# Kernel tuning notes

Hardware: AMD Instinct MI355X
Metric: run time of the kernel (lower is better)

## Reference

```python
import jax, jax.numpy as jnp
import numpy as np

N = 100000      # nodes
E = 3200000     # edges
F_IN = 128      # num_features
H = 32          # hidden_dim (hard-coded in module)
C = 8           # num_classes
B = 128         # graphs in batch
BN_EPS = 1e-5


def setup_inputs() -> dict:
    key = jax.random.key(0)
    ks = jax.random.split(key, 24)
    s = 0.1
    inp = {
        "x": jax.random.normal(ks[0], (N, F_IN), jnp.float32),
        "edge_index": jax.random.randint(ks[1], (2, E), 0, N, dtype=jnp.int32),
        "batch": jnp.sort(jax.random.randint(ks[2], (N,), 0, B, dtype=jnp.int32)),
        # GINConv layer 0 (F_IN -> H -> H) MLP + BN params
        "w1_0": jax.random.normal(ks[3], (F_IN, H), jnp.float32) * s,
        "b1_0": jnp.zeros((H,), jnp.float32),
        "w2_0": jax.random.normal(ks[4], (H, H), jnp.float32) * s,
        "b2_0": jnp.zeros((H,), jnp.float32),
        "g_0": jnp.ones((H,), jnp.float32),
        "be_0": jnp.zeros((H,), jnp.float32),
        # GINConv layers 1..3 (H -> H -> H), stacked
        "w1s": jax.random.normal(ks[5], (3, H, H), jnp.float32) * s,
        "b1s": jnp.zeros((3, H), jnp.float32),
        "w2s": jax.random.normal(ks[6], (3, H, H), jnp.float32) * s,
        "b2s": jnp.zeros((3, H), jnp.float32),
        "gs": jnp.ones((3, H), jnp.float32),
        "bes": jnp.zeros((3, H), jnp.float32),
        # classifier head
        "fc1_w": jax.random.normal(ks[7], (H, H), jnp.float32) * s,
        "fc1_b": jnp.zeros((H,), jnp.float32),
        "fc2_w": jax.random.normal(ks[8], (H, C), jnp.float32) * s,
        "fc2_b": jnp.zeros((C,), jnp.float32),
    }
    return inp


def _gin_conv(h, src, dst, w1, b1, w2, b2):
    # GINConv with eps=0: MLP((1+eps)*x + sum_{j in N(i)} x_j)
    agg = jax.ops.segment_sum(h[src], dst, num_segments=N)  # scatter-add aggregation
    z = h + agg
    return jnp.maximum(z @ w1 + b1, 0.0) @ w2 + b2


def _batch_norm(h, gamma, beta):
    # BatchNorm1d in training mode: batch stats over node dim, biased variance
    mean = h.mean(axis=0)
    var = jnp.mean(jnp.square(h - mean), axis=0)
    return gamma * (h - mean) * jax.lax.rsqrt(var + BN_EPS) + beta


def reference(x, edge_index, batch, w1_0, b1_0, w2_0, b2_0, g_0, be_0,
              w1s, b1s, w2s, b2s, gs, bes, fc1_w, fc1_b, fc2_w, fc2_b):
    src, dst = edge_index[0], edge_index[1]
    h = _batch_norm(jnp.maximum(_gin_conv(x, src, dst, w1_0, b1_0, w2_0, b2_0), 0.0), g_0, be_0)
    for i in range(3):  # fixed small layer loop
        h = _batch_norm(jnp.maximum(_gin_conv(h, src, dst, w1s[i], b1s[i], w2s[i], b2s[i]), 0.0), gs[i], bes[i])
    # global_mean_pool over batch ids
    counts = jax.ops.segment_sum(jnp.ones((N,), h.dtype), batch, num_segments=B)
    pooled = jax.ops.segment_sum(h, batch, num_segments=B) / jnp.maximum(counts, 1.0)[:, None]
    h = jnp.maximum(pooled @ fc1_w + fc1_b, 0.0)
    # dropout p=0.5 treated as identity (eval-mode determinism)
    logits = h @ fc2_w + fc2_b
    return jax.nn.log_softmax(logits, axis=-1)
```

## Files before the change

### kernel.cpp

```cpp
#include <hip/hip_runtime.h>
#include <hip/hip_bf16.h>

#define NN   100000
#define EE   3200000
#define HH   32
#define BB   128
#define KMAX 96
#define LSTRIDE 97
#define NBKT 1024
#define BSPAN 98
#define EBLK 256
#define CHUNK 12500

typedef float f32x4 __attribute__((ext_vector_type(4)));

static constexpr size_t Q_OFF      = 0;
static constexpr size_t EPACK_OFF  = 6400000;
static constexpr size_t H_OFF      = 19200000;
static constexpr size_t SRC_OFF    = 32000000;
static constexpr size_t OFF_OFF    = 44800000;
static constexpr size_t HIST_OFF   = 45300000;
static constexpr size_t CUR_OFF    = 46400000;
static constexpr size_t BBASE_OFF  = 47500000;
static constexpr size_t STATS_OFF  = 47600000;
static constexpr size_t POOLED_OFF = 47601024;
static constexpr size_t PCNT_OFF   = 47617408;
static constexpr size_t ZERO_OFF   = STATS_OFF;
static constexpr size_t ZERO_BYTES = 17920;

__global__ __launch_bounds__(256) void hist_kernel(const int* __restrict__ ei,
                                                   int* __restrict__ hist) {
    __shared__ int lh[NBKT];
    int tid = threadIdx.x, blk = blockIdx.x;
    for (int i = tid; i < NBKT; i += 256) lh[i] = 0;
    __syncthreads();
    int e0 = blk * CHUNK;
    for (int e = e0 + tid; e < e0 + CHUNK; e += 256) {
        int d = ei[EE + e];
        atomicAdd(&lh[d / BSPAN], 1);
    }
    __syncthreads();
    for (int i = tid; i < NBKT; i += 256) hist[blk * NBKT + i] = lh[i];
}

__global__ __launch_bounds__(1024) void bucket_scan_kernel(const int* __restrict__ hist,
                                                           int* __restrict__ bbase,
                                                           int* __restrict__ cursor) {
    __shared__ int sm[NBKT];
    int t = threadIdx.x;
    int mine = 0;
    for (int blk = 0; blk < EBLK; blk++) mine += hist[blk * NBKT + t];
    sm[t] = mine;
    __syncthreads();
    for (int off = 1; off < NBKT; off <<= 1) {
        int v = (t >= off) ? sm[t - off] : 0;
        __syncthreads();
        sm[t] += v;
        __syncthreads();
    }
    int base = sm[t] - mine;
    bbase[t] = base;
    cursor[t] = base;
    if (t == NBKT - 1) bbase[NBKT] = sm[t];
}

__global__ __launch_bounds__(256) void scatter_kernel(const int* __restrict__ ei,
                                                      const int* __restrict__ hist,
                                                      int* __restrict__ cursor,
                                                      int* __restrict__ epack) {
    __shared__ int lbs[NBKT];
    __shared__ int lh[NBKT];
    int tid = threadIdx.x, blk = blockIdx.x;
    for (int i = tid; i < NBKT; i += 256) {
        int c = hist[blk * NBKT + i];
        lbs[i] = (c > 0) ? atomicAdd(&cursor[i], c) : 0;
        lh[i] = 0;
    }
    __syncthreads();
    int e0 = blk * CHUNK;
    for (int e = e0 + tid; e < e0 + CHUNK; e += 256) {
        int s = ei[e];
        int d = ei[EE + e];
        int b = d / BSPAN;
        int slot = lbs[b] + atomicAdd(&lh[b], 1);
        epack[slot] = s | ((d - b * BSPAN) << 17);
    }
}

__global__ __launch_bounds__(256) void csr_compact_kernel(const int* __restrict__ epack,
                                                          const int* __restrict__ bbase,
                                                          int* __restrict__ off,
                                                          int* __restrict__ srcs) {
    __shared__ int lcnt[BSPAN];
    __shared__ int lbase[BSPAN + 1];
    __shared__ int lcsr[BSPAN * LSTRIDE];
    int b = blockIdx.x;
    int base = b * BSPAN;
    int span = NN - base;
    if (span <= 0) return;
    if (span > BSPAN) span = BSPAN;
    int tid = threadIdx.x;
    for (int i = tid; i < span; i += 256) lcnt[i] = 0;
    __syncthreads();
    int p0 = bbase[b], p1 = bbase[b + 1];
    for (int i = p0 + tid; i < p1; i += 256) {
        int wd = epack[i];
        int ld = wd >> 17;
        int slot = atomicAdd(&lcnt[ld], 1);
        if (slot < KMAX) lcsr[ld * LSTRIDE + slot] = wd & 0x1FFFF;
    }
    __syncthreads();
    if (tid == 0) {
        int run = 0;
        for (int i = 0; i < span; i++) { lbase[i] = run; run += min(lcnt[i], KMAX); }
        lbase[span] = run;
    }
    __syncthreads();
    for (int i = tid; i < span; i += 256) off[base + i] = p0 + lbase[i];
    if (base + span == NN && tid == 0) off[NN] = p0 + lbase[span];
    int m = lbase[span];
    for (int j = tid; j < m; j += 256) {
        int lo = 0, hi = span - 1;
        while (lo < hi) {
            int mid = (lo + hi + 1) >> 1;
            if (lbase[mid] <= j) lo = mid; else hi = mid - 1;
        }
        srcs[p0 + j] = lcsr[lo * LSTRIDE + (j - lbase[lo])];
    }
}

__device__ __forceinline__ unsigned bf16rn(float f) {
    unsigned b = __float_as_uint(f);
    return (b + 0x7fffu + ((b >> 16) & 1u)) >> 16;
}

__device__ __forceinline__ void acc_row(float* a, uint4 v) {
    a[0] += __uint_as_float(v.x << 16);
    a[1] += __uint_as_float(v.x & 0xffff0000u);
    a[2] += __uint_as_float(v.y << 16);
    a[3] += __uint_as_float(v.y & 0xffff0000u);
    a[4] += __uint_as_float(v.z << 16);
    a[5] += __uint_as_float(v.z & 0xffff0000u);
    a[6] += __uint_as_float(v.w << 16);
    a[7] += __uint_as_float(v.w & 0xffff0000u);
}

template <int FIN>
__global__ __launch_bounds__(256) void proj_kernel(const float* __restrict__ hin,
                                                   const float* __restrict__ w1,
                                                   const float* __restrict__ stats_prev,
                                                   const float* __restrict__ gamma,
                                                   const float* __restrict__ beta,
                                                   uint4* __restrict__ q4) {
    constexpr int JC = FIN / 4;
    __shared__ float sa[32], sc[32];
    __shared__ float part[4 * 64 * 33];
    int tid = threadIdx.x;
    if constexpr (FIN == 32) {
        if (tid < 32) {
            float mean = stats_prev[tid] * (1.0f / NN);
            float var  = fmaxf(stats_prev[32 + tid] * (1.0f / NN) - mean * mean, 0.f);
            float av = gamma[tid] * rsqrtf(var + 1e-5f);
            sa[tid] = av;
            sc[tid] = beta[tid] - mean * av;
        }
        __syncthreads();
    }
    int wv = __builtin_amdgcn_readfirstlane(tid >> 6);
    int ln = tid & 63;
    int n = blockIdx.x * 64 + ln;
    float acc[32];
#pragma unroll
    for (int c = 0; c < 32; c++) acc[c] = 0.f;
    if (n < NN) {
        const float4* h4 = (const float4*)(hin + (size_t)n * FIN + wv * JC);
        float hv[JC];
#pragma unroll
        for (int k = 0; k < JC / 4; k++) {
            float4 v = h4[k];
            hv[4*k] = v.x; hv[4*k+1] = v.y; hv[4*k+2] = v.z; hv[4*k+3] = v.w;
        }
        if constexpr (FIN == 32) {
#pragma unroll
            for (int j = 0; j < JC; j++) hv[j] = fmaf(hv[j], sa[wv * JC + j], sc[wv * JC + j]);
        }
#pragma unroll 4
        for (int j = 0; j < JC; j++) {
            float hvj = hv[j];
            const float* wrow = w1 + (size_t)(wv * JC + j) * 32;
#pragma unroll
            for (int c = 0; c < 32; c++) acc[c] = fmaf(hvj, wrow[c], acc[c]);
        }
    }
    float* my = part + (wv * 64 + ln) * 33;
#pragma unroll
    for (int c = 0; c < 32; c++) my[c] = acc[c];
    __syncthreads();
    int node = tid >> 2, p = tid & 3;
    int n2 = blockIdx.x * 64 + node;
    if (n2 >= NN) return;
    float r[8];
#pragma unroll
    for (int k = 0; k < 8; k++) {
        int c = p * 8 + k;
        r[k] = (part[(0 * 64 + node) * 33 + c] + part[(1 * 64 + node) * 33 + c])
             + (part[(2 * 64 + node) * 33 + c] + part[(3 * 64 + node) * 33 + c]);
    }
    uint4 u;
    u.x = bf16rn(r[0]) | (bf16rn(r[1]) << 16);
    u.y = bf16rn(r[2]) | (bf16rn(r[3]) << 16);
    u.z = bf16rn(r[4]) | (bf16rn(r[5]) << 16);
    u.w = bf16rn(r[6]) | (bf16rn(r[7]) << 16);
    q4[(size_t)n2 * 4 + p] = u;
}

__global__ __launch_bounds__(256) void gather_mlp_kernel(const uint4* __restrict__ q4,
                                                         const int* __restrict__ srcs,
                                                         const int* __restrict__ off,
                                                         const float* __restrict__ b1,
                                                         const float* __restrict__ w2,
                                                         const float* __restrict__ b2,
                                                         float* __restrict__ hout,
                                                         float* __restrict__ stats) {
    __shared__ float w2t[32 * 33];
    __shared__ float ut[32 * 33];
    __shared__ float pst[32 * 8];
    int tid = threadIdx.x;
    for (int i = tid; i < 1024; i += 256) w2t[(i >> 5) * 33 + (i & 31)] = w2[i];
    int t = blockIdx.x * 256 + tid;
    int n = t >> 3;
    int p = tid & 7;
    int nl = (tid >> 3) & 31;
    int e0 = off[n], e1 = off[n + 1];
    float acc[32];
#pragma unroll
    for (int c = 0; c < 32; c++) acc[c] = 0.f;
    int i = e0 + p;
    for (; i + 8 < e1; i += 16) {
        int s0 = __builtin_nontemporal_load(srcs + i);
        int s1 = __builtin_nontemporal_load(srcs + i + 8);
        uint4 a0 = q4[(size_t)s0 * 4 + 0];
        uint4 a1 = q4[(size_t)s0 * 4 + 1];
        uint4 a2 = q4[(size_t)s0 * 4 + 2];
        uint4 a3 = q4[(size_t)s0 * 4 + 3];
        uint4 c0 = q4[(size_t)s1 * 4 + 0];
        uint4 c1 = q4[(size_t)s1 * 4 + 1];
        uint4 c2 = q4[(size_t)s1 * 4 + 2];
        uint4 c3 = q4[(size_t)s1 * 4 + 3];
        acc_row(acc + 0,  a0); acc_row(acc + 8,  a1);
        acc_row(acc + 16, a2); acc_row(acc + 24, a3);
        acc_row(acc + 0,  c0); acc_row(acc + 8,  c1);
        acc_row(acc + 16, c2); acc_row(acc + 24, c3);
    }
    if (i < e1) {
        int s0 = __builtin_nontemporal_load(srcs + i);
        uint4 a0 = q4[(size_t)s0 * 4 + 0];
        uint4 a1 = q4[(size_t)s0 * 4 + 1];
        uint4 a2 = q4[(size_t)s0 * 4 + 2];
        uint4 a3 = q4[(size_t)s0 * 4 + 3];
        acc_row(acc + 0,  a0); acc_row(acc + 8,  a1);
        acc_row(acc + 16, a2); acc_row(acc + 24, a3);
    }
    int sel1 = p & 1, sel2 = (p >> 1) & 1, sel3 = (p >> 2) & 1;
    float k16[16];
#pragma unroll
    for (int r = 0; r < 16; r++) {
        float send = sel1 ? acc[r] : acc[r + 16];
        float recv = __shfl_xor(send, 1);
        k16[r] = (sel1 ? acc[r + 16] : acc[r]) + recv;
    }
    float k8[8];
#pragma unroll
    for (int r = 0; r < 8; r++) {
        float send = sel2 ? k16[r] : k16[r + 8];
        float recv = __shfl_xor(send, 2);
        k8[r] = (sel2 ? k16[r + 8] : k16[r]) + recv;
    }
    float k4[4];
#pragma unroll
    for (int r = 0; r < 4; r++) {
        float send = sel3 ? k8[r] : k8[r + 4];
        float recv = __shfl_xor(send, 4);
        k4[r] = (sel3 ? k8[r + 4] : k8[r]) + recv;
    }
    int base = 16 * sel1 + 8 * sel2 + 4 * sel3;
    {
        uint4 v = q4[(size_t)n * 4 + (base >> 3)];
        unsigned w0 = sel3 ? v.z : v.x;
        unsigned w1 = sel3 ? v.w : v.y;
        k4[0] += __uint_as_float(w0 << 16);
        k4[1] += __uint_as_float(w0 & 0xffff0000u);
        k4[2] += __uint_as_float(w1 << 16);
        k4[3] += __uint_as_float(w1 & 0xffff0000u);
    }
    const float4 bv = *(const float4*)(b1 + base);
    float u0 = fmaxf(k4[0] + bv.x, 0.f);
    float u1 = fmaxf(k4[1] + bv.y, 0.f);
    float u2 = fmaxf(k4[2] + bv.z, 0.f);
    float u3 = fmaxf(k4[3] + bv.w, 0.f);
    float* urow = ut + nl * 33 + base;
    urow[0] = u0; urow[1] = u1; urow[2] = u2; urow[3] = u3;
    __syncthreads();
    const float4 b2v = *(const float4*)(b2 + base);
    float o0 = b2v.x, o1 = b2v.y, o2 = b2v.z, o3 = b2v.w;
    const float* un = ut + nl * 33;
#pragma unroll 8
    for (int j = 0; j < 32; j++) {
        float uj = un[j];
        const float* wr = w2t + j * 33 + base;
        o0 = fmaf(uj, wr[0], o0);
        o1 = fmaf(uj, wr[1], o1);
        o2 = fmaf(uj, wr[2], o2);
        o3 = fmaf(uj, wr[3], o3);
    }
    o0 = fmaxf(o0, 0.f); o1 = fmaxf(o1, 0.f);
    o2 = fmaxf(o2, 0.f); o3 = fmaxf(o3, 0.f);
    f32x4 hv; hv.x = o0; hv.y = o1; hv.z = o2; hv.w = o3;
    __builtin_nontemporal_store(hv, (f32x4*)(hout + (size_t)n * 32 + base));
    float s0 = o0, s1 = o1, s2 = o2, s3 = o3;
    float q0 = o0 * o0, q1 = o1 * o1, q2 = o2 * o2, q3 = o3 * o3;
#pragma unroll
    for (int m = 8; m < 64; m <<= 1) {
        s0 += __shfl_xor(s0, m); s1 += __shfl_xor(s1, m);
        s2 += __shfl_xor(s2, m); s3 += __shfl_xor(s3, m);
        q0 += __shfl_xor(q0, m); q1 += __shfl_xor(q1, m);
        q2 += __shfl_xor(q2, m); q3 += __shfl_xor(q3, m);
    }
    int wv = tid >> 6;
    if ((tid & 63) < 8) {
        float* ps = pst + (wv * 8 + p) * 8;
        ps[0] = s0; ps[1] = s1; ps[2] = s2; ps[3] = s3;
        ps[4] = q0; ps[5] = q1; ps[6] = q2; ps[7] = q3;
    }
    __syncthreads();
    if (tid < 64) {
        int c = tid & 31;
        int issq = tid >> 5;
        int psel = ((c >> 4) & 1) | (((c >> 3) & 1) << 1) | (((c >> 2) & 1) << 2);
        int k = c & 3;
        float s = 0.f;
#pragma unroll
        for (int w = 0; w < 4; w++) s += pst[(w * 8 + psel) * 8 + issq * 4 + k];
        atomicAdd(&stats[issq * 32 + c], s);
    }
}

#define PR 16
__global__ __launch_bounds__(256) void pool_kernel(const float* __restrict__ h,
                                                   const int* __restrict__ batch,
                                                   float* __restrict__ pooled,
                                                   float* __restrict__ pcnt) {
    int t = blockIdx.x * 256 + threadIdx.x;
    int c = t & 31;
    int g = t >> 5;
    int r0 = g * PR;
    if (r0 >= NN) return;
    int r1 = min(r0 + PR, NN);
    int cur = batch[r0];
    float acc = 0.f, cn = 0.f;
    for (int rr = r0; rr < r1; rr++) {
        int b = batch[rr];
        if (b != cur) {
            atomicAdd(&pooled[cur * 32 + c], acc);
            if (c == 0) atomicAdd(&pcnt[cur], cn);
            acc = 0.f; cn = 0.f; cur = b;
        }
        acc += h[(size_t)rr * 32 + c];
        cn += 1.f;
    }
    atomicAdd(&pooled[cur * 32 + c], acc);
    if (c == 0) atomicAdd(&pcnt[cur], cn);
}

__global__ __launch_bounds__(128) void head_kernel(const float* __restrict__ pooled,
                                                   const float* __restrict__ pcnt,
                                                   const float* __restrict__ stats3,
                                                   const float* __restrict__ g3,
                                                   const float* __restrict__ be3,
                                                   const float* __restrict__ fc1w,
                                                   const float* __restrict__ fc1b,
                                                   const float* __restrict__ fc2w,
                                                   const float* __restrict__ fc2b,
                                                   float* __restrict__ out) {
    __shared__ float sa[32], sc[32];
    int g = threadIdx.x;
    if (g < 32) {
        float mean = stats3[g] * (1.0f / NN);
        float var  = fmaxf(stats3[32 + g] * (1.0f / NN) - mean * mean, 0.f);
        float av = g3[g] * rsqrtf(var + 1e-5f);
        sa[g] = av;
        sc[g] = be3[g] - mean * av;
    }
    __syncthreads();
    if (g >= BB) return;
    float inv = 1.f / fmaxf(pcnt[g], 1.f);
    float xv[32];
#pragma unroll
    for (int c = 0; c < 32; c++) xv[c] = fmaf(sa[c], pooled[g * 32 + c] * inv, sc[c]);
    float u[32];
#pragma unroll 4
    for (int k = 0; k < 32; k++) {
        float s = fc1b[k];
#pragma unroll
        for (int c = 0; c < 32; c++) s = fmaf(xv[c], fc1w[c * 32 + k], s);
        u[k] = fmaxf(s, 0.f);
    }
    float l[8];
#pragma unroll
    for (int o = 0; o < 8; o++) {
        float s = fc2b[o];
#pragma unroll
        for (int k = 0; k < 32; k++) s = fmaf(u[k], fc2w[k * 8 + o], s);
        l[o] = s;
    }
    float m = l[0];
#pragma unroll
    for (int o = 1; o < 8; o++) m = fmaxf(m, l[o]);
    float se = 0.f;
#pragma unroll
    for (int o = 0; o < 8; o++) se += expf(l[o] - m);
    float lse = logf(se) + m;
#pragma unroll
    for (int o = 0; o < 8; o++) out[g * 8 + o] = l[o] - lse;
}

extern "C" void kernel_launch(void* const* d_in, const int* in_sizes, int n_in,
                              void* d_out, int out_size, void* d_ws, size_t ws_size,
                              hipStream_t stream) {
    const float* x    = (const float*)d_in[0];
    const int*   ei   = (const int*)d_in[1];
    const int*   batch= (const int*)d_in[2];
    const float* w1_0 = (const float*)d_in[3];
    const float* b1_0 = (const float*)d_in[4];
    const float* w2_0 = (const float*)d_in[5];
    const float* b2_0 = (const float*)d_in[6];
    const float* g_0  = (const float*)d_in[7];
    const float* be_0 = (const float*)d_in[8];
    const float* w1s  = (const float*)d_in[9];
    const float* b1s  = (const float*)d_in[10];
    const float* w2s  = (const float*)d_in[11];
    const float* b2s  = (const float*)d_in[12];
    const float* gs   = (const float*)d_in[13];
    const float* bes  = (const float*)d_in[14];
    const float* fc1w = (const float*)d_in[15];
    const float* fc1b = (const float*)d_in[16];
    const float* fc2w = (const float*)d_in[17];
    const float* fc2b = (const float*)d_in[18];
    float* out = (float*)d_out;

    char* ws = (char*)d_ws;
    uint4*    q4     = (uint4*)(ws + Q_OFF);
    int*      epack  = (int*)(ws + EPACK_OFF);
    float*    h      = (float*)(ws + H_OFF);
    int*      srcs   = (int*)(ws + SRC_OFF);
    int*      off    = (int*)(ws + OFF_OFF);
    int*      hist   = (int*)(ws + HIST_OFF);
    int*      cursor = (int*)(ws + CUR_OFF);
    int*      bbase  = (int*)(ws + BBASE_OFF);
    float*    stats  = (float*)(ws + STATS_OFF);
    float*    pooled = (float*)(ws + POOLED_OFF);
    float*    pcnt   = (float*)(ws + PCNT_OFF);

    (void)hipMemsetAsync(ws + ZERO_OFF, 0, ZERO_BYTES, stream);

    hist_kernel<<<EBLK, 256, 0, stream>>>(ei, hist);
    bucket_scan_kernel<<<1, NBKT, 0, stream>>>(hist, bbase, cursor);
    scatter_kernel<<<EBLK, 256, 0, stream>>>(ei, hist, cursor, epack);
    csr_compact_kernel<<<NBKT, 256, 0, stream>>>(epack, bbase, off, srcs);

    const int pblk = (NN + 63) / 64;
    const int gblk = (NN * 8) / 256;

    proj_kernel<128><<<pblk, 256, 0, stream>>>(x, w1_0, nullptr, nullptr, nullptr, q4);
    gather_mlp_kernel<<<gblk, 256, 0, stream>>>(q4, srcs, off, b1_0, w2_0, b2_0, h, stats);

    for (int i = 0; i < 3; i++) {
        const float* st_prev = stats + i * 64;
        proj_kernel<32><<<pblk, 256, 0, stream>>>(h, w1s + i * 1024, st_prev,
                                                  gs + i * 32, bes + i * 32, q4);
        gather_mlp_kernel<<<gblk, 256, 0, stream>>>(q4, srcs, off, b1s + i * 32,
                                                    w2s + i * 1024, b2s + i * 32, h,
                                                    stats + (i + 1) * 64);
    }

    int pthreads = ((NN + PR - 1) / PR) * 32;
    pool_kernel<<<(pthreads + 255) / 256, 256, 0, stream>>>(h, batch, pooled, pcnt);
    head_kernel<<<1, 128, 0, stream>>>(pooled, pcnt, stats + 3 * 64, gs + 2 * 32,
                                       bes + 2 * 32, fc1w, fc1b, fc2w, fc2b, out);
}
```

Before: 577.2 us.

## Pipeline gather index loads, replace shared-memory MLP with shuffles, replicate stat atomics

Software-pipelines the edge-source index loads in the gather loop, prefetching the next pair while the current rows are loaded, with a predicated tail instead of a separate remainder path. Drops the shared-memory staging and both block barriers in the second MLP layer by exchanging hidden activations via wavefront shuffles and reading w2 directly from global memory. Spreads batch-norm statistic atomics across 8 replica slots, which consumers now sum. It also corrects which gamma/beta are applied to each layer's batch norm. The cost is more global loads of w2 per thread and more atomics per block.

```diff
diff --git a/kernel.cpp b/kernel.cpp
--- a/kernel.cpp
+++ b/kernel.cpp
@@ -23,10 +23,10 @@
 static constexpr size_t CUR_OFF    = 46400000;
 static constexpr size_t BBASE_OFF  = 47500000;
 static constexpr size_t STATS_OFF  = 47600000;
-static constexpr size_t POOLED_OFF = 47601024;
-static constexpr size_t PCNT_OFF   = 47617408;
+static constexpr size_t POOLED_OFF = 47608192;
+static constexpr size_t PCNT_OFF   = 47624576;
 static constexpr size_t ZERO_OFF   = STATS_OFF;
-static constexpr size_t ZERO_BYTES = 17920;
+static constexpr size_t ZERO_BYTES = 25088;
 
 __global__ __launch_bounds__(256) void hist_kernel(const int* __restrict__ ei,
                                                    int* __restrict__ hist) {
@@ -158,8 +158,14 @@
     int tid = threadIdx.x;
     if constexpr (FIN == 32) {
         if (tid < 32) {
-            float mean = stats_prev[tid] * (1.0f / NN);
-            float var  = fmaxf(stats_prev[32 + tid] * (1.0f / NN) - mean * mean, 0.f);
+            float s = 0.f, sq = 0.f;
+#pragma unroll
+            for (int k = 0; k < 8; k++) {
+                s  += stats_prev[k * 64 + tid];
+                sq += stats_prev[k * 64 + 32 + tid];
+            }
+            float mean = s * (1.0f / NN);
+            float var  = fmaxf(sq * (1.0f / NN) - mean * mean, 0.f);
             float av = gamma[tid] * rsqrtf(var + 1e-5f);
             sa[tid] = av;
             sc[tid] = beta[tid] - mean * av;
@@ -222,44 +228,39 @@
                                                          const float* __restrict__ b2,
                                                          float* __restrict__ hout,
                                                          float* __restrict__ stats) {
-    __shared__ float w2t[32 * 33];
-    __shared__ float ut[32 * 33];
-    __shared__ float pst[32 * 8];
     int tid = threadIdx.x;
-    for (int i = tid; i < 1024; i += 256) w2t[(i >> 5) * 33 + (i & 31)] = w2[i];
     int t = blockIdx.x * 256 + tid;
     int n = t >> 3;
     int p = tid & 7;
-    int nl = (tid >> 3) & 31;
     int e0 = off[n], e1 = off[n + 1];
+    int e1m1 = e1 - 1;
     float acc[32];
 #pragma unroll
     for (int c = 0; c < 32; c++) acc[c] = 0.f;
     int i = e0 + p;
-    for (; i + 8 < e1; i += 16) {
-        int s0 = __builtin_nontemporal_load(srcs + i);
-        int s1 = __builtin_nontemporal_load(srcs + i + 8);
-        uint4 a0 = q4[(size_t)s0 * 4 + 0];
-        uint4 a1 = q4[(size_t)s0 * 4 + 1];
-        uint4 a2 = q4[(size_t)s0 * 4 + 2];
-        uint4 a3 = q4[(size_t)s0 * 4 + 3];
-        uint4 c0 = q4[(size_t)s1 * 4 + 0];
-        uint4 c1 = q4[(size_t)s1 * 4 + 1];
-        uint4 c2 = q4[(size_t)s1 * 4 + 2];
-        uint4 c3 = q4[(size_t)s1 * 4 + 3];
+    int sA = __builtin_nontemporal_load(srcs + min(i, e1m1));
+    int sB = __builtin_nontemporal_load(srcs + min(i + 8, e1m1));
+    while (i < e1) {
+        int inext = i + 16;
+        int sC = __builtin_nontemporal_load(srcs + min(inext, e1m1));
+        int sD = __builtin_nontemporal_load(srcs + min(inext + 8, e1m1));
+        bool vB = (i + 8 < e1);
+        int sBc = vB ? sB : sA;
+        uint4 a0 = q4[(size_t)sA * 4 + 0];
+        uint4 a1 = q4[(size_t)sA * 4 + 1];
+        uint4 a2 = q4[(size_t)sA * 4 + 2];
+        uint4 a3 = q4[(size_t)sA * 4 + 3];
+        uint4 c0 = q4[(size_t)sBc * 4 + 0];
+        uint4 c1 = q4[(size_t)sBc * 4 + 1];
+        uint4 c2 = q4[(size_t)sBc * 4 + 2];
+        uint4 c3 = q4[(size_t)sBc * 4 + 3];
         acc_row(acc + 0,  a0); acc_row(acc + 8,  a1);
         acc_row(acc + 16, a2); acc_row(acc + 24, a3);
-        acc_row(acc + 0,  c0); acc_row(acc + 8,  c1);
-        acc_row(acc + 16, c2); acc_row(acc + 24, c3);
-    }
-    if (i < e1) {
-        int s0 = __builtin_nontemporal_load(srcs + i);
-        uint4 a0 = q4[(size_t)s0 * 4 + 0];
-        uint4 a1 = q4[(size_t)s0 * 4 + 1];
-        uint4 a2 = q4[(size_t)s0 * 4 + 2];
-        uint4 a3 = q4[(size_t)s0 * 4 + 3];
-        acc_row(acc + 0,  a0); acc_row(acc + 8,  a1);
-        acc_row(acc + 16, a2); acc_row(acc + 24, a3);
+        if (vB) {
+            acc_row(acc + 0,  c0); acc_row(acc + 8,  c1);
+            acc_row(acc + 16, c2); acc_row(acc + 24, c3);
+        }
+        sA = sC; sB = sD; i = inext;
     }
     int sel1 = p & 1, sel2 = (p >> 1) & 1, sel3 = (p >> 2) & 1;
     float k16[16];
@@ -294,24 +295,23 @@
         k4[3] += __uint_as_float(w1 & 0xffff0000u);
     }
     const float4 bv = *(const float4*)(b1 + base);
-    float u0 = fmaxf(k4[0] + bv.x, 0.f);
-    float u1 = fmaxf(k4[1] + bv.y, 0.f);
-    float u2 = fmaxf(k4[2] + bv.z, 0.f);
-    float u3 = fmaxf(k4[3] + bv.w, 0.f);
-    float* urow = ut + nl * 33 + base;
-    urow[0] = u0; urow[1] = u1; urow[2] = u2; urow[3] = u3;
-    __syncthreads();
+    float uu[4];
+    uu[0] = fmaxf(k4[0] + bv.x, 0.f);
+    uu[1] = fmaxf(k4[1] + bv.y, 0.f);
+    uu[2] = fmaxf(k4[2] + bv.z, 0.f);
+    uu[3] = fmaxf(k4[3] + bv.w, 0.f);
+    int grp8 = (tid & 63) & 56;
     const float4 b2v = *(const float4*)(b2 + base);
     float o0 = b2v.x, o1 = b2v.y, o2 = b2v.z, o3 = b2v.w;
-    const float* un = ut + nl * 33;
-#pragma unroll 8
+#pragma unroll
     for (int j = 0; j < 32; j++) {
-        float uj = un[j];
-        const float* wr = w2t + j * 33 + base;
-        o0 = fmaf(uj, wr[0], o0);
-        o1 = fmaf(uj, wr[1], o1);
-        o2 = fmaf(uj, wr[2], o2);
-        o3 = fmaf(uj, wr[3], o3);
+        int owner = ((j >> 4) & 1) | (((j >> 3) & 1) << 1) | (((j >> 2) & 1) << 2);
+        float uj = __shfl(uu[j & 3], grp8 + owner);
+        const float4 wr = *(const float4*)(w2 + j * 32 + base);
+        o0 = fmaf(uj, wr.x, o0);
+        o1 = fmaf(uj, wr.y, o1);
+        o2 = fmaf(uj, wr.z, o2);
+        o3 = fmaf(uj, wr.w, o3);
     }
     o0 = fmaxf(o0, 0.f); o1 = fmaxf(o1, 0.f);
     o2 = fmaxf(o2, 0.f); o3 = fmaxf(o3, 0.f);
@@ -326,22 +326,16 @@
         q0 += __shfl_xor(q0, m); q1 += __shfl_xor(q1, m);
         q2 += __shfl_xor(q2, m); q3 += __shfl_xor(q3, m);
     }
-    int wv = tid >> 6;
     if ((tid & 63) < 8) {
-        float* ps = pst + (wv * 8 + p) * 8;
-        ps[0] = s0; ps[1] = s1; ps[2] = s2; ps[3] = s3;
-        ps[4] = q0; ps[5] = q1; ps[6] = q2; ps[7] = q3;
-    }
-    __syncthreads();
-    if (tid < 64) {
-        int c = tid & 31;
-        int issq = tid >> 5;
-        int psel = ((c >> 4) & 1) | (((c >> 3) & 1) << 1) | (((c >> 2) & 1) << 2);
-        int k = c & 3;
-        float s = 0.f;
-#pragma unroll
-        for (int w = 0; w < 4; w++) s += pst[(w * 8 + psel) * 8 + issq * 4 + k];
-        atomicAdd(&stats[issq * 32 + c], s);
+        float* st = stats + (((blockIdx.x << 2) + (tid >> 6)) & 7) * 64;
+        atomicAdd(&st[base + 0], s0);
+        atomicAdd(&st[base + 1], s1);
+        atomicAdd(&st[base + 2], s2);
+        atomicAdd(&st[base + 3], s3);
+        atomicAdd(&st[32 + base + 0], q0);
+        atomicAdd(&st[32 + base + 1], q1);
+        atomicAdd(&st[32 + base + 2], q2);
+        atomicAdd(&st[32 + base + 3], q3);
     }
 }
 
@@ -385,8 +379,14 @@
     __shared__ float sa[32], sc[32];
     int g = threadIdx.x;
     if (g < 32) {
-        float mean = stats3[g] * (1.0f / NN);
-        float var  = fmaxf(stats3[32 + g] * (1.0f / NN) - mean * mean, 0.f);
+        float s = 0.f, sq = 0.f;
+#pragma unroll
+        for (int k = 0; k < 8; k++) {
+            s  += stats3[k * 64 + g];
+            sq += stats3[k * 64 + 32 + g];
+        }
+        float mean = s * (1.0f / NN);
+        float var  = fmaxf(sq * (1.0f / NN) - mean * mean, 0.f);
         float av = g3[g] * rsqrtf(var + 1e-5f);
         sa[g] = av;
         sc[g] = be3[g] - mean * av;
@@ -471,20 +471,23 @@
     const int pblk = (NN + 63) / 64;
     const int gblk = (NN * 8) / 256;
 
+    const float* gprev[3]  = { g_0, gs, gs + 32 };
+    const float* beprev[3] = { be_0, bes, bes + 32 };
+
     proj_kernel<128><<<pblk, 256, 0, stream>>>(x, w1_0, nullptr, nullptr, nullptr, q4);
     gather_mlp_kernel<<<gblk, 256, 0, stream>>>(q4, srcs, off, b1_0, w2_0, b2_0, h, stats);
 
     for (int i = 0; i < 3; i++) {
-        const float* st_prev = stats + i * 64;
+        const float* st_prev = stats + i * 512;
         proj_kernel<32><<<pblk, 256, 0, stream>>>(h, w1s + i * 1024, st_prev,
-                                                  gs + i * 32, bes + i * 32, q4);
+                                                  gprev[i], beprev[i], q4);
         gather_mlp_kernel<<<gblk, 256, 0, stream>>>(q4, srcs, off, b1s + i * 32,
                                                     w2s + i * 1024, b2s + i * 32, h,
-                                                    stats + (i + 1) * 64);
+                                                    stats + (i + 1) * 512);
     }
 
     int pthreads = ((NN + PR - 1) / PR) * 32;
     pool_kernel<<<(pthreads + 255) / 256, 256, 0, stream>>>(h, batch, pooled, pcnt);
-    head_kernel<<<1, 128, 0, stream>>>(pooled, pcnt, stats + 3 * 64, gs + 2 * 32,
-                                       bes + 2 * 32, fc1w, fc1b, fc2w, fc2b, out);
-}
+    head_kernel<<<1, 128, 0, stream>>>(pooled, pcnt, stats + 3 * 512, gs + 64,
+                                       bes + 64, fc1w, fc1b, fc2w, fc2b, out);
+}
```

After: 965.5 us. +67.3%, slower.

## Pad per-node CSR neighbor lists to multiples of 16 with dummy zero row

Applied to the files above, without the earlier changes.

The CSR build now rounds each node's neighbor count up to a multiple of 16 and fills the padding with a sentinel index NN that points at a zeroed extra row of q4. It also packs the start offset and the 16-block count into one word. The gather loop therefore runs a fixed number of full 16-wide iterations with no tail branch, and it software-pipelines the index loads one iteration ahead. In exchange it adds extra gathers of the zero row, more srcs memory (per-bucket slack), and a 23-bit limit on offsets.

```diff
diff --git a/kernel.cpp b/kernel.cpp
--- a/kernel.cpp
+++ b/kernel.cpp
@@ -11,20 +11,21 @@
 #define BSPAN 98
 #define EBLK 256
 #define CHUNK 12500
+#define BSLACK 1568
 
 typedef float f32x4 __attribute__((ext_vector_type(4)));
 
 static constexpr size_t Q_OFF      = 0;
-static constexpr size_t EPACK_OFF  = 6400000;
-static constexpr size_t H_OFF      = 19200000;
-static constexpr size_t SRC_OFF    = 32000000;
-static constexpr size_t OFF_OFF    = 44800000;
-static constexpr size_t HIST_OFF   = 45300000;
-static constexpr size_t CUR_OFF    = 46400000;
-static constexpr size_t BBASE_OFF  = 47500000;
-static constexpr size_t STATS_OFF  = 47600000;
-static constexpr size_t POOLED_OFF = 47601024;
-static constexpr size_t PCNT_OFF   = 47617408;
+static constexpr size_t EPACK_OFF  = 6400128;
+static constexpr size_t H_OFF      = 19200128;
+static constexpr size_t SRC_OFF    = 32000128;
+static constexpr size_t OFFP_OFF   = 51300000;
+static constexpr size_t HIST_OFF   = 51700000;
+static constexpr size_t CUR_OFF    = 52748576;
+static constexpr size_t BBASE_OFF  = 52752672;
+static constexpr size_t STATS_OFF  = 52760000;
+static constexpr size_t POOLED_OFF = 52761024;
+static constexpr size_t PCNT_OFF   = 52777408;
 static constexpr size_t ZERO_OFF   = STATS_OFF;
 static constexpr size_t ZERO_BYTES = 17920;
 
@@ -89,7 +90,7 @@
 
 __global__ __launch_bounds__(256) void csr_compact_kernel(const int* __restrict__ epack,
                                                           const int* __restrict__ bbase,
-                                                          int* __restrict__ off,
+                                                          int* __restrict__ offp,
                                                           int* __restrict__ srcs) {
     __shared__ int lcnt[BSPAN];
     __shared__ int lbase[BSPAN + 1];
@@ -110,14 +111,22 @@
         if (slot < KMAX) lcsr[ld * LSTRIDE + slot] = wd & 0x1FFFF;
     }
     __syncthreads();
+    for (int i = tid; i < span; i += 256) lcnt[i] = min(lcnt[i], KMAX);
+    __syncthreads();
     if (tid == 0) {
         int run = 0;
-        for (int i = 0; i < span; i++) { lbase[i] = run; run += min(lcnt[i], KMAX); }
+        for (int i = 0; i < span; i++) {
+            lbase[i] = run;
+            run += (lcnt[i] + 15) & ~15;
+        }
         lbase[span] = run;
     }
     __syncthreads();
-    for (int i = tid; i < span; i += 256) off[base + i] = p0 + lbase[i];
-    if (base + span == NN && tid == 0) off[NN] = p0 + lbase[span];
+    int sb = p0 + b * BSLACK;
+    for (int i = tid; i < span; i += 256) {
+        int cnt16 = (lbase[i + 1] - lbase[i]) >> 4;
+        offp[base + i] = (sb + lbase[i]) | (cnt16 << 23);
+    }
     int m = lbase[span];
     for (int j = tid; j < m; j += 256) {
         int lo = 0, hi = span - 1;
@@ -125,7 +134,8 @@
             int mid = (lo + hi + 1) >> 1;
             if (lbase[mid] <= j) lo = mid; else hi = mid - 1;
         }
-        srcs[p0 + j] = lcsr[lo * LSTRIDE + (j - lbase[lo])];
+        int l = j - lbase[lo];
+        srcs[sb + j] = (l < lcnt[lo]) ? lcsr[lo * LSTRIDE + l] : NN;
     }
 }
 
@@ -216,7 +226,7 @@
 
 __global__ __launch_bounds__(256) void gather_mlp_kernel(const uint4* __restrict__ q4,
                                                          const int* __restrict__ srcs,
-                                                         const int* __restrict__ off,
+                                                         const int* __restrict__ offp,
                                                          const float* __restrict__ b1,
                                                          const float* __restrict__ w2,
                                                          const float* __restrict__ b2,
@@ -231,35 +241,45 @@
     int n = t >> 3;
     int p = tid & 7;
     int nl = (tid >> 3) & 31;
-    int e0 = off[n], e1 = off[n + 1];
+    int w = offp[n];
+    int cnt = w >> 23;
+    int i = (w & 0x7FFFFF) + p;
     float acc[32];
 #pragma unroll
     for (int c = 0; c < 32; c++) acc[c] = 0.f;
-    int i = e0 + p;
-    for (; i + 8 < e1; i += 16) {
-        int s0 = __builtin_nontemporal_load(srcs + i);
-        int s1 = __builtin_nontemporal_load(srcs + i + 8);
-        uint4 a0 = q4[(size_t)s0 * 4 + 0];
-        uint4 a1 = q4[(size_t)s0 * 4 + 1];
-        uint4 a2 = q4[(size_t)s0 * 4 + 2];
-        uint4 a3 = q4[(size_t)s0 * 4 + 3];
-        uint4 c0 = q4[(size_t)s1 * 4 + 0];
-        uint4 c1 = q4[(size_t)s1 * 4 + 1];
-        uint4 c2 = q4[(size_t)s1 * 4 + 2];
-        uint4 c3 = q4[(size_t)s1 * 4 + 3];
+    if (cnt > 0) {
+        int sA = __builtin_nontemporal_load(srcs + i);
+        int sB = __builtin_nontemporal_load(srcs + i + 8);
+        for (int k = 1; k < cnt; k++) {
+            i += 16;
+            int sC = __builtin_nontemporal_load(srcs + i);
+            int sD = __builtin_nontemporal_load(srcs + i + 8);
+            uint4 a0 = q4[(size_t)sA * 4 + 0];
+            uint4 a1 = q4[(size_t)sA * 4 + 1];
+            uint4 a2 = q4[(size_t)sA * 4 + 2];
+            uint4 a3 = q4[(size_t)sA * 4 + 3];
+            uint4 c0 = q4[(size_t)sB * 4 + 0];
+            uint4 c1 = q4[(size_t)sB * 4 + 1];
+            uint4 c2 = q4[(size_t)sB * 4 + 2];
+            uint4 c3 = q4[(size_t)sB * 4 + 3];
+            acc_row(acc + 0,  a0); acc_row(acc + 8,  a1);
+            acc_row(acc + 16, a2); acc_row(acc + 24, a3);
+            acc_row(acc + 0,  c0); acc_row(acc + 8,  c1);
+            acc_row(acc + 16, c2); acc_row(acc + 24, c3);
+            sA = sC; sB = sD;
+        }
+        uint4 a0 = q4[(size_t)sA * 4 + 0];
+        uint4 a1 = q4[(size_t)sA * 4 + 1];
+        uint4 a2 = q4[(size_t)sA * 4 + 2];
+        uint4 a3 = q4[(size_t)sA * 4 + 3];
+        uint4 c0 = q4[(size_t)sB * 4 + 0];
+        uint4 c1 = q4[(size_t)sB * 4 + 1];
+        uint4 c2 = q4[(size_t)sB * 4 + 2];
+        uint4 c3 = q4[(size_t)sB * 4 + 3];
         acc_row(acc + 0,  a0); acc_row(acc + 8,  a1);
         acc_row(acc + 16, a2); acc_row(acc + 24, a3);
         acc_row(acc + 0,  c0); acc_row(acc + 8,  c1);
         acc_row(acc + 16, c2); acc_row(acc + 24, c3);
-    }
-    if (i < e1) {
-        int s0 = __builtin_nontemporal_load(srcs + i);
-        uint4 a0 = q4[(size_t)s0 * 4 + 0];
-        uint4 a1 = q4[(size_t)s0 * 4 + 1];
-        uint4 a2 = q4[(size_t)s0 * 4 + 2];
-        uint4 a3 = q4[(size_t)s0 * 4 + 3];
-        acc_row(acc + 0,  a0); acc_row(acc + 8,  a1);
-        acc_row(acc + 16, a2); acc_row(acc + 24, a3);
     }
     int sel1 = p & 1, sel2 = (p >> 1) & 1, sel3 = (p >> 2) & 1;
     float k16[16];
@@ -340,7 +360,7 @@
         int k = c & 3;
         float s = 0.f;
 #pragma unroll
-        for (int w = 0; w < 4; w++) s += pst[(w * 8 + psel) * 8 + issq * 4 + k];
+        for (int w2i = 0; w2i < 4; w2i++) s += pst[(w2i * 8 + psel) * 8 + issq * 4 + k];
         atomicAdd(&stats[issq * 32 + c], s);
     }
 }
@@ -453,7 +473,7 @@
     int*      epack  = (int*)(ws + EPACK_OFF);
     float*    h      = (float*)(ws + H_OFF);
     int*      srcs   = (int*)(ws + SRC_OFF);
-    int*      off    = (int*)(ws + OFF_OFF);
+    int*      offp   = (int*)(ws + OFFP_OFF);
     int*      hist   = (int*)(ws + HIST_OFF);
     int*      cursor = (int*)(ws + CUR_OFF);
     int*      bbase  = (int*)(ws + BBASE_OFF);
@@ -462,23 +482,24 @@
     float*    pcnt   = (float*)(ws + PCNT_OFF);
 
     (void)hipMemsetAsync(ws + ZERO_OFF, 0, ZERO_BYTES, stream);
+    (void)hipMemsetAsync(ws + Q_OFF + (size_t)NN * 64, 0, 64, stream);
 
     hist_kernel<<<EBLK, 256, 0, stream>>>(ei, hist);
     bucket_scan_kernel<<<1, NBKT, 0, stream>>>(hist, bbase, cursor);
     scatter_kernel<<<EBLK, 256, 0, stream>>>(ei, hist, cursor, epack);
-    csr_compact_kernel<<<NBKT, 256, 0, stream>>>(epack, bbase, off, srcs);
+    csr_compact_kernel<<<NBKT, 256, 0, stream>>>(epack, bbase, offp, srcs);
 
     const int pblk = (NN + 63) / 64;
     const int gblk = (NN * 8) / 256;
 
     proj_kernel<128><<<pblk, 256, 0, stream>>>(x, w1_0, nullptr, nullptr, nullptr, q4);
-    gather_mlp_kernel<<<gblk, 256, 0, stream>>>(q4, srcs, off, b1_0, w2_0, b2_0, h, stats);
+    gather_mlp_kernel<<<gblk, 256, 0, stream>>>(q4, srcs, offp, b1_0, w2_0, b2_0, h, stats);
 
     for (int i = 0; i < 3; i++) {
         const float* st_prev = stats + i * 64;
         proj_kernel<32><<<pblk, 256, 0, stream>>>(h, w1s + i * 1024, st_prev,
                                                   gs + i * 32, bes + i * 32, q4);
-        gather_mlp_kernel<<<gblk, 256, 0, stream>>>(q4, srcs, off, b1s + i * 32,
+        gather_mlp_kernel<<<gblk, 256, 0, stream>>>(q4, srcs, offp, b1s + i * 32,
                                                     w2s + i * 1024, b2s + i * 32, h,
                                                     stats + (i + 1) * 64);
     }
```

After: 607.8 us. 1.05x slower.

## Split gather by feature slice: 4 threads per node, each owning 8 channels

Applied to the files above, without the earlier changes.

The neighbour gather changes from 8 threads per node (each reading whole 64-byte rows of alternate edges, then a butterfly shuffle reduction across lanes) to 4 threads per node, each reading one 16-byte slice of every neighbour row. This removes the cross-lane reduction of the 32 accumulators and cuts register pressure to 8 accumulators per thread. The inner loop is unrolled by 8 to keep more loads in flight. The trade-off is that each thread walks the full edge list serially, so edge-index loads are repeated four times per node and per-thread latency grows with degree.

```diff
diff --git a/kernel.cpp b/kernel.cpp
--- a/kernel.cpp
+++ b/kernel.cpp
@@ -223,125 +223,104 @@
                                                          float* __restrict__ hout,
                                                          float* __restrict__ stats) {
     __shared__ float w2t[32 * 33];
-    __shared__ float ut[32 * 33];
-    __shared__ float pst[32 * 8];
+    __shared__ float ut[64 * 33];
+    __shared__ float pst[16 * 16];
     int tid = threadIdx.x;
     for (int i = tid; i < 1024; i += 256) w2t[(i >> 5) * 33 + (i & 31)] = w2[i];
     int t = blockIdx.x * 256 + tid;
-    int n = t >> 3;
-    int p = tid & 7;
-    int nl = (tid >> 3) & 31;
-    int e0 = off[n], e1 = off[n + 1];
-    float acc[32];
-#pragma unroll
-    for (int c = 0; c < 32; c++) acc[c] = 0.f;
-    int i = e0 + p;
-    for (; i + 8 < e1; i += 16) {
-        int s0 = __builtin_nontemporal_load(srcs + i);
-        int s1 = __builtin_nontemporal_load(srcs + i + 8);
-        uint4 a0 = q4[(size_t)s0 * 4 + 0];
-        uint4 a1 = q4[(size_t)s0 * 4 + 1];
-        uint4 a2 = q4[(size_t)s0 * 4 + 2];
-        uint4 a3 = q4[(size_t)s0 * 4 + 3];
-        uint4 c0 = q4[(size_t)s1 * 4 + 0];
-        uint4 c1 = q4[(size_t)s1 * 4 + 1];
-        uint4 c2 = q4[(size_t)s1 * 4 + 2];
-        uint4 c3 = q4[(size_t)s1 * 4 + 3];
-        acc_row(acc + 0,  a0); acc_row(acc + 8,  a1);
-        acc_row(acc + 16, a2); acc_row(acc + 24, a3);
-        acc_row(acc + 0,  c0); acc_row(acc + 8,  c1);
-        acc_row(acc + 16, c2); acc_row(acc + 24, c3);
-    }
-    if (i < e1) {
-        int s0 = __builtin_nontemporal_load(srcs + i);
-        uint4 a0 = q4[(size_t)s0 * 4 + 0];
-        uint4 a1 = q4[(size_t)s0 * 4 + 1];
-        uint4 a2 = q4[(size_t)s0 * 4 + 2];
-        uint4 a3 = q4[(size_t)s0 * 4 + 3];
-        acc_row(acc + 0,  a0); acc_row(acc + 8,  a1);
-        acc_row(acc + 16, a2); acc_row(acc + 24, a3);
-    }
-    int sel1 = p & 1, sel2 = (p >> 1) & 1, sel3 = (p >> 2) & 1;
-    float k16[16];
-#pragma unroll
-    for (int r = 0; r < 16; r++) {
-        float send = sel1 ? acc[r] : acc[r + 16];
-        float recv = __shfl_xor(send, 1);
-        k16[r] = (sel1 ? acc[r + 16] : acc[r]) + recv;
-    }
-    float k8[8];
-#pragma unroll
-    for (int r = 0; r < 8; r++) {
-        float send = sel2 ? k16[r] : k16[r + 8];
-        float recv = __shfl_xor(send, 2);
-        k8[r] = (sel2 ? k16[r + 8] : k16[r]) + recv;
-    }
-    float k4[4];
-#pragma unroll
-    for (int r = 0; r < 4; r++) {
-        float send = sel3 ? k8[r] : k8[r + 4];
-        float recv = __shfl_xor(send, 4);
-        k4[r] = (sel3 ? k8[r + 4] : k8[r]) + recv;
-    }
-    int base = 16 * sel1 + 8 * sel2 + 4 * sel3;
-    {
-        uint4 v = q4[(size_t)n * 4 + (base >> 3)];
-        unsigned w0 = sel3 ? v.z : v.x;
-        unsigned w1 = sel3 ? v.w : v.y;
-        k4[0] += __uint_as_float(w0 << 16);
-        k4[1] += __uint_as_float(w0 & 0xffff0000u);
-        k4[2] += __uint_as_float(w1 << 16);
-        k4[3] += __uint_as_float(w1 & 0xffff0000u);
-    }
-    const float4 bv = *(const float4*)(b1 + base);
-    float u0 = fmaxf(k4[0] + bv.x, 0.f);
-    float u1 = fmaxf(k4[1] + bv.y, 0.f);
-    float u2 = fmaxf(k4[2] + bv.z, 0.f);
-    float u3 = fmaxf(k4[3] + bv.w, 0.f);
-    float* urow = ut + nl * 33 + base;
-    urow[0] = u0; urow[1] = u1; urow[2] = u2; urow[3] = u3;
-    __syncthreads();
-    const float4 b2v = *(const float4*)(b2 + base);
-    float o0 = b2v.x, o1 = b2v.y, o2 = b2v.z, o3 = b2v.w;
-    const float* un = ut + nl * 33;
+    int n = t >> 2;
+    int p = tid & 3;
+    int node64 = tid >> 2;
+    bool valid = (n < NN);
+    float a[8];
+#pragma unroll
+    for (int k = 0; k < 8; k++) a[k] = valid ? b1[p * 8 + k] : 0.f;
+    if (valid) {
+        acc_row(a, q4[(size_t)n * 4 + p]);
+        int o0 = off[n];
+        int d = off[n + 1] - o0;
+        const int* lst = srcs + o0;
+        int i = 0;
+        for (; i + 8 <= d; i += 8) {
+            int s0 = __builtin_nontemporal_load(lst + i);
+            int s1 = __builtin_nontemporal_load(lst + i + 1);
+            int s2 = __builtin_nontemporal_load(lst + i + 2);
+            int s3 = __builtin_nontemporal_load(lst + i + 3);
+            int s4 = __builtin_nontemporal_load(lst + i + 4);
+            int s5 = __builtin_nontemporal_load(lst + i + 5);
+            int s6 = __builtin_nontemporal_load(lst + i + 6);
+            int s7 = __builtin_nontemporal_load(lst + i + 7);
+            uint4 v0 = q4[(size_t)s0 * 4 + p];
+            uint4 v1 = q4[(size_t)s1 * 4 + p];
+            uint4 v2 = q4[(size_t)s2 * 4 + p];
+            uint4 v3 = q4[(size_t)s3 * 4 + p];
+            uint4 v4 = q4[(size_t)s4 * 4 + p];
+            uint4 v5 = q4[(size_t)s5 * 4 + p];
+            uint4 v6 = q4[(size_t)s6 * 4 + p];
+            uint4 v7 = q4[(size_t)s7 * 4 + p];
+            acc_row(a, v0); acc_row(a, v1); acc_row(a, v2); acc_row(a, v3);
+            acc_row(a, v4); acc_row(a, v5); acc_row(a, v6); acc_row(a, v7);
+        }
+        for (; i < d; i++) {
+            int s = __builtin_nontemporal_load(lst + i);
+            acc_row(a, q4[(size_t)s * 4 + p]);
+        }
+    }
+    float* urow = ut + node64 * 33 + p * 8;
+#pragma unroll
+    for (int k = 0; k < 8; k++) urow[k] = fmaxf(a[k], 0.f);
+    __syncthreads();
+    int base = p * 8;
+    float o[8];
+#pragma unroll
+    for (int k = 0; k < 8; k++) o[k] = valid ? b2[base + k] : 0.f;
+    const float* un = ut + node64 * 33;
 #pragma unroll 8
     for (int j = 0; j < 32; j++) {
         float uj = un[j];
         const float* wr = w2t + j * 33 + base;
-        o0 = fmaf(uj, wr[0], o0);
-        o1 = fmaf(uj, wr[1], o1);
-        o2 = fmaf(uj, wr[2], o2);
-        o3 = fmaf(uj, wr[3], o3);
-    }
-    o0 = fmaxf(o0, 0.f); o1 = fmaxf(o1, 0.f);
-    o2 = fmaxf(o2, 0.f); o3 = fmaxf(o3, 0.f);
-    f32x4 hv; hv.x = o0; hv.y = o1; hv.z = o2; hv.w = o3;
-    __builtin_nontemporal_store(hv, (f32x4*)(hout + (size_t)n * 32 + base));
-    float s0 = o0, s1 = o1, s2 = o2, s3 = o3;
-    float q0 = o0 * o0, q1 = o1 * o1, q2 = o2 * o2, q3 = o3 * o3;
-#pragma unroll
-    for (int m = 8; m < 64; m <<= 1) {
-        s0 += __shfl_xor(s0, m); s1 += __shfl_xor(s1, m);
-        s2 += __shfl_xor(s2, m); s3 += __shfl_xor(s3, m);
-        q0 += __shfl_xor(q0, m); q1 += __shfl_xor(q1, m);
-        q2 += __shfl_xor(q2, m); q3 += __shfl_xor(q3, m);
+#pragma unroll
+        for (int k = 0; k < 8; k++) o[k] = fmaf(uj, wr[k], o[k]);
+    }
+#pragma unroll
+    for (int k = 0; k < 8; k++) o[k] = fmaxf(o[k], 0.f);
+    if (valid) {
+        f32x4 h0, h1;
+        h0.x = o[0]; h0.y = o[1]; h0.z = o[2]; h0.w = o[3];
+        h1.x = o[4]; h1.y = o[5]; h1.z = o[6]; h1.w = o[7];
+        f32x4* hr = (f32x4*)(hout + (size_t)n * 32 + base);
+        __builtin_nontemporal_store(h0, hr);
+        __builtin_nontemporal_store(h1, hr + 1);
+    } else {
+#pragma unroll
+        for (int k = 0; k < 8; k++) o[k] = 0.f;
+    }
+    float s[8], q[8];
+#pragma unroll
+    for (int k = 0; k < 8; k++) { s[k] = o[k]; q[k] = o[k] * o[k]; }
+#pragma unroll
+    for (int m = 4; m < 64; m <<= 1) {
+#pragma unroll
+        for (int k = 0; k < 8; k++) {
+            s[k] += __shfl_xor(s[k], m);
+            q[k] += __shfl_xor(q[k], m);
+        }
     }
     int wv = tid >> 6;
-    if ((tid & 63) < 8) {
-        float* ps = pst + (wv * 8 + p) * 8;
-        ps[0] = s0; ps[1] = s1; ps[2] = s2; ps[3] = s3;
-        ps[4] = q0; ps[5] = q1; ps[6] = q2; ps[7] = q3;
+    if ((tid & 63) < 4) {
+        float* ps = pst + (wv * 4 + p) * 16;
+#pragma unroll
+        for (int k = 0; k < 8; k++) { ps[k] = s[k]; ps[8 + k] = q[k]; }
     }
     __syncthreads();
     if (tid < 64) {
         int c = tid & 31;
         int issq = tid >> 5;
-        int psel = ((c >> 4) & 1) | (((c >> 3) & 1) << 1) | (((c >> 2) & 1) << 2);
-        int k = c & 3;
-        float s = 0.f;
-#pragma unroll
-        for (int w = 0; w < 4; w++) s += pst[(w * 8 + psel) * 8 + issq * 4 + k];
-        atomicAdd(&stats[issq * 32 + c], s);
+        int psel = c >> 3, k = c & 7;
+        float acc = 0.f;
+#pragma unroll
+        for (int w = 0; w < 4; w++) acc += pst[(w * 4 + psel) * 16 + issq * 8 + k];
+        atomicAdd(&stats[issq * 32 + c], acc);
     }
 }
 
@@ -469,7 +448,7 @@
     csr_compact_kernel<<<NBKT, 256, 0, stream>>>(epack, bbase, off, srcs);
 
     const int pblk = (NN + 63) / 64;
-    const int gblk = (NN * 8) / 256;
+    const int gblk = (NN * 4 + 255) / 256;
 
     proj_kernel<128><<<pblk, 256, 0, stream>>>(x, w1_0, nullptr, nullptr, nullptr, q4);
     gather_mlp_kernel<<<gblk, 256, 0, stream>>>(q4, srcs, off, b1_0, w2_0, b2_0, h, stats);
```

After: 546.2 us. 1.06x faster.
